# Performance work log

Measured on AMD Instinct MI355X. Metric: run time of the kernel, lower is better.

The kernel has to match this reference:

```python
import jax, jax.numpy as jnp
import numpy as np

P = 131072
S = 64
EMAP_H, EMAP_W = 512, 1024
EPS = 1e-12

def _normalize(x):
    return x / jnp.maximum(jnp.linalg.norm(x, axis=-1, keepdims=True), EPS)

def _construct_tbn(normal):
    # rows = tangent, bitangent, normal -> world-to-local rotation
    up = jnp.broadcast_to(jnp.array([0.0, 1.0, 0.0], normal.dtype), normal.shape)
    tangent = _normalize(jnp.cross(up, normal))
    degen = (normal[..., 0] ** 2 + normal[..., 2] ** 2) <= 0.0
    tangent = jnp.where(degen[..., None], jnp.array([1.0, 0.0, 0.0], normal.dtype), tangent)
    bitangent = _normalize(jnp.cross(normal, tangent))
    return jnp.stack([tangent, bitangent, normal], axis=-2)  # [P,3,3]

def _latlong_uv(d):
    u = 0.5 * (1.0 + jnp.arctan2(d[..., 0], -d[..., 2]) / jnp.pi)
    v = jnp.arccos(jnp.clip(d[..., 1], -1.0, 1.0)) / jnp.pi
    return jnp.stack([u, v], axis=-1)

def _reflect(i, n):
    return _normalize(-i + 2.0 * jnp.sum(i * n, axis=-1, keepdims=True) * n)

def _sample_ggx_vndf(v_local, alpha, u1, u2):
    a3 = jnp.concatenate([alpha, alpha, jnp.ones_like(alpha)], axis=-1)  # [P,3]
    vh = _normalize(v_local * a3)
    ln = jnp.broadcast_to(jnp.array([0.0, 0.0, 1.0], vh.dtype), vh.shape)
    b1 = _normalize(jnp.cross(ln, vh))
    degen = jnp.linalg.norm(vh[:, :2], axis=-1) <= 0.0
    b1 = jnp.where(degen[:, None], jnp.array([1.0, 0.0, 0.0], vh.dtype), b1)
    b2 = _normalize(jnp.cross(vh, b1))
    r = jnp.sqrt(u1)
    theta = 2.0 * jnp.pi * u2
    t1 = r * jnp.cos(theta)
    t2 = r * jnp.sin(theta)
    s = 0.5 * (1.0 + vh[:, 2:3])
    t2 = (1.0 - s) * jnp.sqrt(1.0 - t1 ** 2) + s * t2
    t3 = jnp.sqrt(jnp.clip(1.0 - t1 ** 2 - t2 ** 2, 0.0, 1.0))
    mh = (t1[..., None] * b1[:, None, :] + t2[..., None] * b2[:, None, :]
          + t3[..., None] * vh[:, None, :])
    return _normalize(mh * a3[:, None, :])  # [P,S,3]

def _grid_sample_border(img, grid):
    # img: [3,H,W]; grid: [...,2] in [-1,1]; bilinear, align_corners=False, border pad
    H, W = img.shape[1], img.shape[2]
    x = ((grid[..., 0] + 1.0) * W - 1.0) * 0.5
    y = ((grid[..., 1] + 1.0) * H - 1.0) * 0.5
    x0f = jnp.floor(x); y0f = jnp.floor(y)
    wx = x - x0f; wy = y - y0f
    x0 = jnp.clip(x0f.astype(jnp.int32), 0, W - 1)
    x1 = jnp.clip(x0f.astype(jnp.int32) + 1, 0, W - 1)
    y0 = jnp.clip(y0f.astype(jnp.int32), 0, H - 1)
    y1 = jnp.clip(y0f.astype(jnp.int32) + 1, 0, H - 1)
    v00 = img[:, y0, x0]; v01 = img[:, y0, x1]
    v10 = img[:, y1, x0]; v11 = img[:, y1, x1]
    out = (v00 * (1 - wx) * (1 - wy) + v01 * wx * (1 - wy)
           + v10 * (1 - wx) * wy + v11 * wx * wy)
    return jnp.moveaxis(out, 0, -1)  # [...,3]

def _smith(alpha, cos):
    a2 = alpha ** 2
    return 2.0 * cos / (cos + jnp.sqrt(a2 + (1.0 - a2) * cos ** 2))

def _forward(emap, view_dir, normal, albedo, roughness, metalness, u1, u2, uc, vc):
    img = emap[0]  # [3,H,W]
    alpha = roughness ** 2
    tbn = _construct_tbn(normal)  # [P,3,3]
    v_local = jnp.einsum('pij,pj->pi', tbn, view_dir)
    m_local = _sample_ggx_vndf(v_local, alpha, u1, u2)       # [P,S,3]
    m_world = jnp.einsum('pji,psj->psi', tbn, m_local)       # tbn^T @ m
    light = _reflect(view_dir[:, None, :], m_world)          # [P,S,3]
    rad = _grid_sample_border(img, _latlong_uv(light) * 2.0 - 1.0)  # [P,S,3]
    # specular (metal) shading
    half = _normalize(view_dir[:, None, :] + light)
    hdv = jnp.clip(jnp.sum(half * view_dir[:, None, :], axis=-1), 0.0, 1.0)
    ndv = jnp.clip(jnp.sum(normal[:, None, :] * view_dir[:, None, :], axis=-1), 0.0, 1.0)
    ndl = jnp.clip(jnp.sum(normal[:, None, :] * light, axis=-1), 0.0, 1.0)
    f0 = metalness * albedo + (1.0 - metalness) * 0.04       # [P,3]
    fresnel = f0[:, None, :] + (1.0 - f0[:, None, :]) * (1.0 - hdv[..., None]) ** 5
    geometric = _smith(alpha, ndv) * _smith(alpha, ndl)
    smith_view = jnp.clip(_smith(alpha, ndv), 1e-10, 1.0)
    spec = jnp.mean(fresnel * geometric[..., None] * rad / smith_view[..., None], axis=1)
    # diffuse: cosine-hemisphere sampling + Lambert
    phi = 2.0 * jnp.pi * uc
    ct = jnp.sqrt(vc); st = jnp.sqrt(1.0 - vc)
    ld_local = jnp.stack([jnp.cos(phi) * st, jnp.sin(phi) * st, ct], axis=-1)
    ld = jnp.einsum('pji,psj->psi', tbn, ld_local)
    rad_d = _grid_sample_border(img, _latlong_uv(ld) * 2.0 - 1.0)
    kd = albedo * (1.0 - metalness)
    diff = jnp.mean(rad_d * kd[:, None, :], axis=1)
    return spec + diff  # [P,3]

def setup_inputs() -> dict:
    key = jax.random.key(0)
    ks = jax.random.split(key, 10)
    view_dir = _normalize(jax.random.normal(ks[0], (P, 3), jnp.float32))
    normal = _normalize(jax.random.normal(ks[1], (P, 3), jnp.float32))
    albedo = jax.random.uniform(ks[2], (P, 3), jnp.float32)
    roughness = 0.05 + 0.9 * jax.random.uniform(ks[3], (P, 1), jnp.float32)
    metalness = jax.random.uniform(ks[4], (P, 1), jnp.float32)
    emap = jax.random.uniform(ks[5], (1, 3, EMAP_H, EMAP_W), jnp.float32) * 2.0
    u1 = jax.random.uniform(ks[6], (P, S), jnp.float32)
    u2 = jax.random.uniform(ks[7], (P, S), jnp.float32)
    uc = jax.random.uniform(ks[8], (P, S), jnp.float32)
    vc = jax.random.uniform(ks[9], (P, S), jnp.float32)
    return {"emap": emap, "view_dir": view_dir, "normal": normal, "albedo": albedo,
            "roughness": roughness, "metalness": metalness,
            "u1": u1, "u2": u2, "uc": uc, "vc": vc}

def reference(emap, view_dir, normal, albedo, roughness, metalness, u1, u2, uc, vc):
    return _forward(emap, view_dir, normal, albedo, roughness, metalness, u1, u2, uc, vc)
```

## Files before the change

### kernel.cpp

```cpp
#include <hip/hip_runtime.h>
#include <math.h>

namespace {

constexpr int PN = 131072;
constexpr int SN = 64;
constexpr int EH = 512;
constexpr int EW = 1024;
constexpr float SPI = 162.97466172610083f;

struct F3 { float x, y, z; };

__device__ __forceinline__ float dot3(F3 a, F3 b) { return a.x*b.x + a.y*b.y + a.z*b.z; }
__device__ __forceinline__ F3 cross3(F3 a, F3 b) {
    return F3{a.y*b.z - a.z*b.y, a.z*b.x - a.x*b.z, a.x*b.y - a.y*b.x};
}
__device__ __forceinline__ float clampf(float x, float lo, float hi) {
    return fminf(fmaxf(x, lo), hi);
}
__device__ __forceinline__ F3 norm3(F3 a) {
    float l2 = a.x*a.x + a.y*a.y + a.z*a.z;
    float inv = __builtin_amdgcn_rsqf(fmaxf(l2, 1e-24f));
    return F3{a.x*inv, a.y*inv, a.z*inv};
}
__device__ __forceinline__ float smithf(float alpha, float c) {
    float a2 = alpha*alpha;
    float den = c + __builtin_amdgcn_sqrtf(a2 + (1.0f - a2)*c*c);
    return 2.0f*c*__builtin_amdgcn_rcpf(den);
}

__device__ __forceinline__ float fast_atan2(float y, float x) {
    float ax = fabsf(x), ay = fabsf(y);
    float mx = fmaxf(ax, ay), mn = fminf(ax, ay);
    float a = mn * __builtin_amdgcn_rcpf(mx);
    if (mx == 0.0f) a = 0.0f;
    float s = a*a;
    float p = fmaf(s, -0.01172120f, 0.05265332f);
    p = fmaf(s, p, -0.11643287f);
    p = fmaf(s, p,  0.19354346f);
    p = fmaf(s, p, -0.33262347f);
    p = fmaf(s, p,  0.99997726f);
    float r = p * a;
    if (ay > ax)  r = 1.57079632679f - r;
    if (x < 0.0f) r = 3.14159265359f - r;
    return copysignf(r, y);
}

__device__ __forceinline__ float fast_acos(float x) {
    float ax = fabsf(x);
    float p = fmaf(ax, -0.0012624911f, 0.0066700901f);
    p = fmaf(ax, p, -0.0170881256f);
    p = fmaf(ax, p,  0.0308918810f);
    p = fmaf(ax, p, -0.0501743046f);
    p = fmaf(ax, p,  0.0889789874f);
    p = fmaf(ax, p, -0.2145988016f);
    p = fmaf(ax, p,  1.5707963050f);
    float s = __builtin_amdgcn_sqrtf(fmaxf(1.0f - ax, 0.0f));
    float r = s * p;
    return (x >= 0.0f) ? r : 3.14159265359f - r;
}

__device__ __forceinline__ void env_addr(F3 d, int& i0, int& i1,
                                         float& wx, float& wy,
                                         bool& at_l, bool& at_r) {
    float t  = fast_atan2(d.x, -d.z);
    float vv = fast_acos(clampf(d.y, -1.0f, 1.0f));
    float x = fmaf(t,  SPI, 511.5f);
    float y = fmaf(vv, SPI, -0.5f);
    float x0f = floorf(x), y0f = floorf(y);
    wx = x - x0f; wy = y - y0f;
    int ix = (int)x0f, iy = (int)y0f;
    int xb = min(max(ix, 0), EW - 2);
    int y0 = min(max(iy, 0), EH - 1);
    int y1 = min(max(iy + 1, 0), EH - 1);
    at_l = ix < 0;
    at_r = ix >= EW - 1;
    i0 = (y0 << 10) + xb;
    i1 = (y1 << 10) + xb;
}

__device__ __forceinline__ void rgb9e5_addmul(unsigned int v, float w, F3& acc) {
    float scale = __uint_as_float(((v >> 27) + 103u) << 23);
    float ws = w * scale;
    acc.x = fmaf((float)(v & 511u), ws, acc.x);
    acc.y = fmaf((float)((v >> 9) & 511u), ws, acc.y);
    acc.z = fmaf((float)((v >> 18) & 511u), ws, acc.z);
}

__device__ __forceinline__ F3 env_blend9(uint2 r0, uint2 r1, float wx, float wy,
                                         bool at_l, bool at_r) {
    unsigned int t00 = at_r ? r0.y : r0.x;
    unsigned int t01 = at_l ? r0.x : r0.y;
    unsigned int t10 = at_r ? r1.y : r1.x;
    unsigned int t11 = at_l ? r1.x : r1.y;
    float w00 = (1.0f - wx)*(1.0f - wy);
    float w01 = wx*(1.0f - wy);
    float w10 = (1.0f - wx)*wy;
    float w11 = wx*wy;
    F3 acc{0.0f, 0.0f, 0.0f};
    rgb9e5_addmul(t00, w00, acc);
    rgb9e5_addmul(t01, w01, acc);
    rgb9e5_addmul(t10, w10, acc);
    rgb9e5_addmul(t11, w11, acc);
    return acc;
}

template<int CTRL, int ROW_MASK, bool BC>
__device__ __forceinline__ float dpp_add_step(float x) {
    int ti = __builtin_amdgcn_update_dpp(0, __float_as_int(x), CTRL, ROW_MASK, 0xf, BC);
    return x + __int_as_float(ti);
}
__device__ __forceinline__ float wave_sum(float x) {
    x = dpp_add_step<0x111, 0xf, true >(x);
    x = dpp_add_step<0x112, 0xf, true >(x);
    x = dpp_add_step<0x114, 0xf, true >(x);
    x = dpp_add_step<0x118, 0xf, true >(x);
    x = dpp_add_step<0x142, 0xa, false>(x);
    x = dpp_add_step<0x143, 0xc, false>(x);
    return __int_as_float(__builtin_amdgcn_readlane(__float_as_int(x), 63));
}

__global__ void relayout_kernel(const float* __restrict__ img, unsigned int* __restrict__ tex) {
    int i = blockIdx.x*blockDim.x + threadIdx.x;
    const int HW = EH*EW;
    if (i < HW) {
        float r = img[i], g = img[HW + i], b = img[2*HW + i];
        float m = fmaxf(fmaxf(r, g), b);
        int es = min(max((int)(__float_as_uint(m) >> 23) - 111, 0), 31);
        float sc = __uint_as_float((unsigned int)(151 - es) << 23);
        unsigned int R = min(511u, (unsigned int)rintf(r*sc));
        unsigned int G = min(511u, (unsigned int)rintf(g*sc));
        unsigned int B = min(511u, (unsigned int)rintf(b*sc));
        tex[i] = ((unsigned int)es << 27) | (B << 18) | (G << 9) | R;
    }
}

template<bool TEX>
__global__ __launch_bounds__(256) void ibl_kernel(
    const float* __restrict__ emap, const unsigned int* __restrict__ tex,
    const float* __restrict__ view_dir, const float* __restrict__ normal,
    const float* __restrict__ albedo, const float* __restrict__ rough_,
    const float* __restrict__ metal_, const float* __restrict__ u1_,
    const float* __restrict__ u2_, const float* __restrict__ uc_,
    const float* __restrict__ vc_, float* __restrict__ out)
{
    int lane = threadIdx.x & 63;
    int wid  = (blockIdx.x << 2) + (threadIdx.x >> 6);
    int p0   = __builtin_amdgcn_readfirstlane(wid << 1);

    float U1[2], U2[2], UC[2], VC[2];
    F3 v[2], n[2], f0[2], kd[2];
    float alpha[2];
    #pragma unroll
    for (int k = 0; k < 2; ++k) {
        int p = p0 + k;
        size_t si = (size_t)p*SN + lane;
        U1[k] = __builtin_nontemporal_load(u1_ + si);
        U2[k] = __builtin_nontemporal_load(u2_ + si);
        UC[k] = __builtin_nontemporal_load(uc_ + si);
        VC[k] = __builtin_nontemporal_load(vc_ + si);
        v[k]   = F3{view_dir[3*p], view_dir[3*p+1], view_dir[3*p+2]};
        n[k]   = F3{normal[3*p],   normal[3*p+1],   normal[3*p+2]};
        F3 alb = F3{albedo[3*p],   albedo[3*p+1],   albedo[3*p+2]};
        float rg = rough_[p];
        alpha[k] = rg*rg;
        float metal = metal_[p];
        f0[k] = F3{metal*alb.x + (1.0f - metal)*0.04f,
                   metal*alb.y + (1.0f - metal)*0.04f,
                   metal*alb.z + (1.0f - metal)*0.04f};
        kd[k] = F3{alb.x*(1.0f - metal), alb.y*(1.0f - metal), alb.z*(1.0f - metal)};
    }

    F3 t[2], b[2];
    #pragma unroll
    for (int k = 0; k < 2; ++k) {
        float nx2nz2 = n[k].x*n[k].x + n[k].z*n[k].z;
        if (nx2nz2 <= 0.0f) t[k] = F3{1.0f, 0.0f, 0.0f};
        else                t[k] = norm3(F3{n[k].z, 0.0f, -n[k].x});
        b[k] = cross3(n[k], t[k]);
    }

    uint2 dr0[2], dr1[2];
    float dwx[2], dwy[2];
    bool d_l[2], d_r[2];
    F3 ld[2];
    #pragma unroll
    for (int k = 0; k < 2; ++k) {
        float sph = __builtin_amdgcn_sinf(UC[k]);
        float cph = __builtin_amdgcn_cosf(UC[k]);
        float ct = __builtin_amdgcn_sqrtf(VC[k]);
        float st = __builtin_amdgcn_sqrtf(fmaxf(1.0f - VC[k], 0.0f));
        F3 ldl = F3{cph*st, sph*st, ct};
        ld[k] = F3{t[k].x*ldl.x + b[k].x*ldl.y + n[k].x*ldl.z,
                   t[k].y*ldl.x + b[k].y*ldl.y + n[k].y*ldl.z,
                   t[k].z*ldl.x + b[k].z*ldl.y + n[k].z*ldl.z};
        if (TEX) {
            int i0, i1;
            env_addr(ld[k], i0, i1, dwx[k], dwy[k], d_l[k], d_r[k]);
            dr0[k] = *reinterpret_cast<const uint2*>(tex + i0);
            dr1[k] = *reinterpret_cast<const uint2*>(tex + i1);
        }
    }

    uint2 sr0[2], sr1[2];
    float swx[2], swy[2];
    bool s_l[2], s_r[2];
    F3 light[2];
    float sv_ratio[2];
    #pragma unroll
    for (int k = 0; k < 2; ++k) {
        F3 vl = F3{dot3(t[k], v[k]), dot3(b[k], v[k]), dot3(n[k], v[k])};
        float ndv = clampf(vl.z, 0.0f, 1.0f);
        float s_ndv = smithf(alpha[k], ndv);
        float inv_sv = __builtin_amdgcn_rcpf(clampf(s_ndv, 1e-10f, 1.0f));
        sv_ratio[k] = s_ndv * inv_sv;

        F3 vh = norm3(F3{vl.x*alpha[k], vl.y*alpha[k], vl.z});
        F3 b1;
        float l2d = vh.x*vh.x + vh.y*vh.y;
        if (l2d <= 0.0f) b1 = F3{1.0f, 0.0f, 0.0f};
        else             b1 = norm3(F3{-vh.y, vh.x, 0.0f});
        F3 b2 = cross3(vh, b1);
        float sfac = 0.5f*(1.0f + vh.z);

        float r = __builtin_amdgcn_sqrtf(U1[k]);
        float sth = __builtin_amdgcn_sinf(U2[k]);
        float cth = __builtin_amdgcn_cosf(U2[k]);
        float t1 = r*cth;
        float t2 = r*sth;
        t2 = (1.0f - sfac)*__builtin_amdgcn_sqrtf(fmaxf(1.0f - t1*t1, 0.0f)) + sfac*t2;
        float t3 = __builtin_amdgcn_sqrtf(clampf(1.0f - t1*t1 - t2*t2, 0.0f, 1.0f));
        F3 mh = F3{t1*b1.x + t2*b2.x + t3*vh.x,
                   t1*b1.y + t2*b2.y + t3*vh.y,
                   t1*b1.z + t2*b2.z + t3*vh.z};
        F3 ml = norm3(F3{mh.x*alpha[k], mh.y*alpha[k], mh.z});
        F3 m = F3{t[k].x*ml.x + b[k].x*ml.y + n[k].x*ml.z,
                  t[k].y*ml.x + b[k].y*ml.y + n[k].y*ml.z,
                  t[k].z*ml.x + b[k].z*ml.y + n[k].z*ml.z};
        float idm = dot3(v[k], m);
        light[k] = F3{fmaf(2.0f*idm, m.x, -v[k].x),
                      fmaf(2.0f*idm, m.y, -v[k].y),
                      fmaf(2.0f*idm, m.z, -v[k].z)};
        if (TEX) {
            int i0, i1;
            env_addr(light[k], i0, i1, swx[k], swy[k], s_l[k], s_r[k]);
            sr0[k] = *reinterpret_cast<const uint2*>(tex + i0);
            sr1[k] = *reinterpret_cast<const uint2*>(tex + i1);
        }
    }

    float fresc[2];
    float om5[2];
    #pragma unroll
    for (int k = 0; k < 2; ++k) {
        F3 hlf = norm3(F3{v[k].x + light[k].x, v[k].y + light[k].y, v[k].z + light[k].z});
        float hdv = clampf(dot3(hlf, v[k]), 0.0f, 1.0f);
        float ndl = clampf(dot3(n[k], light[k]), 0.0f, 1.0f);
        float s_ndl = smithf(alpha[k], ndl);
        fresc[k] = sv_ratio[k] * s_ndl;
        float om = 1.0f - hdv;
        float om2 = om*om;
        om5[k] = om2*om2*om;
    }

    #pragma unroll
    for (int k = 0; k < 2; ++k) {
        F3 rad, radd;
        if (TEX) {
            radd = env_blend9(dr0[k], dr1[k], dwx[k], dwy[k], d_l[k], d_r[k]);
            rad  = env_blend9(sr0[k], sr1[k], swx[k], swy[k], s_l[k], s_r[k]);
        } else {
            const int HW = EH*EW;
            #pragma unroll
            for (int pass = 0; pass < 2; ++pass) {
                F3 d = pass ? light[k] : ld[k];
                int i0, i1; float wx, wy; bool atl, atr;
                env_addr(d, i0, i1, wx, wy, atl, atr);
                int x0 = atr ? 1 : 0, x1 = atl ? 0 : 1;
                F3 o;
                float* po = &o.x;
                #pragma unroll
                for (int c = 0; c < 3; ++c) {
                    const float* pl = emap + c*HW;
                    float v00 = pl[i0 + x0], v01 = pl[i0 + x1];
                    float v10 = pl[i1 + x0], v11 = pl[i1 + x1];
                    float rr0 = fmaf(wx, v01 - v00, v00);
                    float rr1 = fmaf(wx, v11 - v10, v10);
                    po[c] = fmaf(wy, rr1 - rr0, rr0);
                }
                if (pass) rad = o; else radd = o;
            }
        }
        float gs = fresc[k];
        F3 acc;
        acc.x = fmaf((f0[k].x + (1.0f - f0[k].x)*om5[k])*gs, rad.x, radd.x*kd[k].x);
        acc.y = fmaf((f0[k].y + (1.0f - f0[k].y)*om5[k])*gs, rad.y, radd.y*kd[k].y);
        acc.z = fmaf((f0[k].z + (1.0f - f0[k].z)*om5[k])*gs, rad.z, radd.z*kd[k].z);

        float sx = wave_sum(acc.x);
        float sy = wave_sum(acc.y);
        float sz = wave_sum(acc.z);

        if (lane == 0) {
            const float inv_s = 1.0f/(float)SN;
            int p = p0 + k;
            __builtin_nontemporal_store(sx*inv_s, out + 3*p + 0);
            __builtin_nontemporal_store(sy*inv_s, out + 3*p + 1);
            __builtin_nontemporal_store(sz*inv_s, out + 3*p + 2);
        }
    }
}

}

extern "C" void kernel_launch(void* const* d_in, const int* in_sizes, int n_in,
                              void* d_out, int out_size, void* d_ws, size_t ws_size,
                              hipStream_t stream) {
    const float* emap     = (const float*)d_in[0];
    const float* view_dir = (const float*)d_in[1];
    const float* normal   = (const float*)d_in[2];
    const float* albedo   = (const float*)d_in[3];
    const float* rough    = (const float*)d_in[4];
    const float* metal    = (const float*)d_in[5];
    const float* u1       = (const float*)d_in[6];
    const float* u2       = (const float*)d_in[7];
    const float* uc       = (const float*)d_in[8];
    const float* vc       = (const float*)d_in[9];
    float* out            = (float*)d_out;

    const int HW = EH*EW;
    const size_t tex_bytes = (size_t)HW*sizeof(unsigned int);
    const int main_blocks = PN/8;

    if (ws_size >= tex_bytes) {
        unsigned int* tex = (unsigned int*)d_ws;
        relayout_kernel<<<(HW + 255)/256, 256, 0, stream>>>(emap, tex);
        ibl_kernel<true><<<main_blocks, 256, 0, stream>>>(
            emap, tex, view_dir, normal, albedo, rough, metal, u1, u2, uc, vc, out);
    } else {
        ibl_kernel<false><<<main_blocks, 256, 0, stream>>>(
            emap, nullptr, view_dir, normal, albedo, rough, metal, u1, u2, uc, vc, out);
    }
}
```

Baseline: 153.5 us.

## Process four points per wave and simplify shading math

Each wave now handles four points instead of two, which halves the grid size and gives more independent texture gathers in flight per wave to hide memory latency. The half-vector normalization is replaced by a closed-form half-angle identity, the Smith ratio clamp is turned into a select, and tangent normalization uses one rsq. The wave reduction now writes from lane 63 instead of doing a readlane, and f0/kd are computed late to shorten register live ranges. More points per wave raises register pressure and may cut occupancy.

```diff
diff --git a/kernel.cpp b/kernel.cpp
--- a/kernel.cpp
+++ b/kernel.cpp
@@ -7,6 +7,7 @@
 constexpr int SN = 64;
 constexpr int EH = 512;
 constexpr int EW = 1024;
+constexpr int KP = 4;
 constexpr float SPI = 162.97466172610083f;
 
 struct F3 { float x, y, z; };
@@ -110,14 +111,14 @@
     int ti = __builtin_amdgcn_update_dpp(0, __float_as_int(x), CTRL, ROW_MASK, 0xf, BC);
     return x + __int_as_float(ti);
 }
-__device__ __forceinline__ float wave_sum(float x) {
+__device__ __forceinline__ float wave_sum63(float x) {
     x = dpp_add_step<0x111, 0xf, true >(x);
     x = dpp_add_step<0x112, 0xf, true >(x);
     x = dpp_add_step<0x114, 0xf, true >(x);
     x = dpp_add_step<0x118, 0xf, true >(x);
     x = dpp_add_step<0x142, 0xa, false>(x);
     x = dpp_add_step<0x143, 0xc, false>(x);
-    return __int_as_float(__builtin_amdgcn_readlane(__float_as_int(x), 63));
+    return x;
 }
 
 __global__ void relayout_kernel(const float* __restrict__ img, unsigned int* __restrict__ tex) {
@@ -146,13 +147,13 @@
 {
     int lane = threadIdx.x & 63;
     int wid  = (blockIdx.x << 2) + (threadIdx.x >> 6);
-    int p0   = __builtin_amdgcn_readfirstlane(wid << 1);
-
-    float U1[2], U2[2], UC[2], VC[2];
-    F3 v[2], n[2], f0[2], kd[2];
-    float alpha[2];
-    #pragma unroll
-    for (int k = 0; k < 2; ++k) {
+    int p0   = __builtin_amdgcn_readfirstlane(wid * KP);
+
+    float U1[KP], U2[KP], UC[KP], VC[KP];
+    F3 v[KP], n[KP], alb[KP];
+    float alpha[KP], metal[KP];
+    #pragma unroll
+    for (int k = 0; k < KP; ++k) {
         int p = p0 + k;
         size_t si = (size_t)p*SN + lane;
         U1[k] = __builtin_nontemporal_load(u1_ + si);
@@ -161,31 +162,28 @@
         VC[k] = __builtin_nontemporal_load(vc_ + si);
         v[k]   = F3{view_dir[3*p], view_dir[3*p+1], view_dir[3*p+2]};
         n[k]   = F3{normal[3*p],   normal[3*p+1],   normal[3*p+2]};
-        F3 alb = F3{albedo[3*p],   albedo[3*p+1],   albedo[3*p+2]};
+        alb[k] = F3{albedo[3*p],   albedo[3*p+1],   albedo[3*p+2]};
         float rg = rough_[p];
         alpha[k] = rg*rg;
-        float metal = metal_[p];
-        f0[k] = F3{metal*alb.x + (1.0f - metal)*0.04f,
-                   metal*alb.y + (1.0f - metal)*0.04f,
-                   metal*alb.z + (1.0f - metal)*0.04f};
-        kd[k] = F3{alb.x*(1.0f - metal), alb.y*(1.0f - metal), alb.z*(1.0f - metal)};
-    }
-
-    F3 t[2], b[2];
-    #pragma unroll
-    for (int k = 0; k < 2; ++k) {
+        metal[k] = metal_[p];
+    }
+
+    F3 t[KP], b[KP];
+    #pragma unroll
+    for (int k = 0; k < KP; ++k) {
         float nx2nz2 = n[k].x*n[k].x + n[k].z*n[k].z;
+        float invt = __builtin_amdgcn_rsqf(nx2nz2);
         if (nx2nz2 <= 0.0f) t[k] = F3{1.0f, 0.0f, 0.0f};
-        else                t[k] = norm3(F3{n[k].z, 0.0f, -n[k].x});
+        else                t[k] = F3{n[k].z*invt, 0.0f, -n[k].x*invt};
         b[k] = cross3(n[k], t[k]);
     }
 
-    uint2 dr0[2], dr1[2];
-    float dwx[2], dwy[2];
-    bool d_l[2], d_r[2];
-    F3 ld[2];
-    #pragma unroll
-    for (int k = 0; k < 2; ++k) {
+    uint2 dr0[KP], dr1[KP];
+    float dwx[KP], dwy[KP];
+    bool d_l[KP], d_r[KP];
+    F3 ld[KP];
+    #pragma unroll
+    for (int k = 0; k < KP; ++k) {
         float sph = __builtin_amdgcn_sinf(UC[k]);
         float cph = __builtin_amdgcn_cosf(UC[k]);
         float ct = __builtin_amdgcn_sqrtf(VC[k]);
@@ -202,24 +200,24 @@
         }
     }
 
-    uint2 sr0[2], sr1[2];
-    float swx[2], swy[2];
-    bool s_l[2], s_r[2];
-    F3 light[2];
-    float sv_ratio[2];
-    #pragma unroll
-    for (int k = 0; k < 2; ++k) {
+    uint2 sr0[KP], sr1[KP];
+    float swx[KP], swy[KP];
+    bool s_l[KP], s_r[KP];
+    F3 light[KP];
+    float sv_ratio[KP];
+    #pragma unroll
+    for (int k = 0; k < KP; ++k) {
         F3 vl = F3{dot3(t[k], v[k]), dot3(b[k], v[k]), dot3(n[k], v[k])};
         float ndv = clampf(vl.z, 0.0f, 1.0f);
         float s_ndv = smithf(alpha[k], ndv);
-        float inv_sv = __builtin_amdgcn_rcpf(clampf(s_ndv, 1e-10f, 1.0f));
-        sv_ratio[k] = s_ndv * inv_sv;
+        sv_ratio[k] = (s_ndv >= 1e-10f) ? 1.0f : s_ndv * 1e10f;
 
         F3 vh = norm3(F3{vl.x*alpha[k], vl.y*alpha[k], vl.z});
         F3 b1;
         float l2d = vh.x*vh.x + vh.y*vh.y;
+        float invb = __builtin_amdgcn_rsqf(l2d);
         if (l2d <= 0.0f) b1 = F3{1.0f, 0.0f, 0.0f};
-        else             b1 = norm3(F3{-vh.y, vh.x, 0.0f});
+        else             b1 = F3{-vh.y*invb, vh.x*invb, 0.0f};
         F3 b2 = cross3(vh, b1);
         float sfac = 0.5f*(1.0f + vh.z);
 
@@ -249,12 +247,12 @@
         }
     }
 
-    float fresc[2];
-    float om5[2];
-    #pragma unroll
-    for (int k = 0; k < 2; ++k) {
-        F3 hlf = norm3(F3{v[k].x + light[k].x, v[k].y + light[k].y, v[k].z + light[k].z});
-        float hdv = clampf(dot3(hlf, v[k]), 0.0f, 1.0f);
+    float fresc[KP];
+    float om5[KP];
+    #pragma unroll
+    for (int k = 0; k < KP; ++k) {
+        float c = dot3(v[k], light[k]);
+        float hdv = __builtin_amdgcn_sqrtf(clampf(0.5f + 0.5f*c, 0.0f, 1.0f));
         float ndl = clampf(dot3(n[k], light[k]), 0.0f, 1.0f);
         float s_ndl = smithf(alpha[k], ndl);
         fresc[k] = sv_ratio[k] * s_ndl;
@@ -264,7 +262,7 @@
     }
 
     #pragma unroll
-    for (int k = 0; k < 2; ++k) {
+    for (int k = 0; k < KP; ++k) {
         F3 rad, radd;
         if (TEX) {
             radd = env_blend9(dr0[k], dr1[k], dwx[k], dwy[k], d_l[k], d_r[k]);
@@ -292,16 +290,21 @@
             }
         }
         float gs = fresc[k];
+        float mt = metal[k];
+        F3 f0 = F3{mt*alb[k].x + (1.0f - mt)*0.04f,
+                   mt*alb[k].y + (1.0f - mt)*0.04f,
+                   mt*alb[k].z + (1.0f - mt)*0.04f};
+        F3 kd = F3{alb[k].x*(1.0f - mt), alb[k].y*(1.0f - mt), alb[k].z*(1.0f - mt)};
         F3 acc;
-        acc.x = fmaf((f0[k].x + (1.0f - f0[k].x)*om5[k])*gs, rad.x, radd.x*kd[k].x);
-        acc.y = fmaf((f0[k].y + (1.0f - f0[k].y)*om5[k])*gs, rad.y, radd.y*kd[k].y);
-        acc.z = fmaf((f0[k].z + (1.0f - f0[k].z)*om5[k])*gs, rad.z, radd.z*kd[k].z);
-
-        float sx = wave_sum(acc.x);
-        float sy = wave_sum(acc.y);
-        float sz = wave_sum(acc.z);
-
-        if (lane == 0) {
+        acc.x = fmaf((f0.x + (1.0f - f0.x)*om5[k])*gs, rad.x, radd.x*kd.x);
+        acc.y = fmaf((f0.y + (1.0f - f0.y)*om5[k])*gs, rad.y, radd.y*kd.y);
+        acc.z = fmaf((f0.z + (1.0f - f0.z)*om5[k])*gs, rad.z, radd.z*kd.z);
+
+        float sx = wave_sum63(acc.x);
+        float sy = wave_sum63(acc.y);
+        float sz = wave_sum63(acc.z);
+
+        if (lane == 63) {
             const float inv_s = 1.0f/(float)SN;
             int p = p0 + k;
             __builtin_nontemporal_store(sx*inv_s, out + 3*p + 0);
@@ -330,7 +333,7 @@
 
     const int HW = EH*EW;
     const size_t tex_bytes = (size_t)HW*sizeof(unsigned int);
-    const int main_blocks = PN/8;
+    const int main_blocks = PN/(4*KP);
 
     if (ws_size >= tex_bytes) {
         unsigned int* tex = (unsigned int*)d_ws;
```

Result: slower. 160.5 us (+4.6%).

## Split fused IBL kernel into separate diffuse and specular passes

Applied to the files above, without the earlier changes.

Splits the single fused kernel into a diffuse kernel that writes the output and a specular kernel that adds into it, so each pass uses fewer registers and has a smaller texture working set. It also simplifies math: the half-vector dot product is computed via the cosine half-angle identity, the shadowing ratio is made branchy instead of using a reciprocal, and the wave reduction reads its result from lane 63 directly, dropping the readlane. The cost is a second launch, per-point inputs (normal, albedo, metal) being reloaded, and a read-modify-write of the output.

```diff
diff --git a/kernel.cpp b/kernel.cpp
--- a/kernel.cpp
+++ b/kernel.cpp
@@ -105,19 +105,38 @@
     return acc;
 }
 
+__device__ __forceinline__ F3 env_sample_f32(const float* __restrict__ emap, F3 d) {
+    const int HW = EH*EW;
+    int i0, i1; float wx, wy; bool atl, atr;
+    env_addr(d, i0, i1, wx, wy, atl, atr);
+    int x0 = atr ? 1 : 0, x1 = atl ? 0 : 1;
+    F3 o;
+    float* po = &o.x;
+    #pragma unroll
+    for (int c = 0; c < 3; ++c) {
+        const float* pl = emap + c*HW;
+        float v00 = pl[i0 + x0], v01 = pl[i0 + x1];
+        float v10 = pl[i1 + x0], v11 = pl[i1 + x1];
+        float rr0 = fmaf(wx, v01 - v00, v00);
+        float rr1 = fmaf(wx, v11 - v10, v10);
+        po[c] = fmaf(wy, rr1 - rr0, rr0);
+    }
+    return o;
+}
+
 template<int CTRL, int ROW_MASK, bool BC>
 __device__ __forceinline__ float dpp_add_step(float x) {
     int ti = __builtin_amdgcn_update_dpp(0, __float_as_int(x), CTRL, ROW_MASK, 0xf, BC);
     return x + __int_as_float(ti);
 }
-__device__ __forceinline__ float wave_sum(float x) {
+__device__ __forceinline__ float wave_sum63(float x) {
     x = dpp_add_step<0x111, 0xf, true >(x);
     x = dpp_add_step<0x112, 0xf, true >(x);
     x = dpp_add_step<0x114, 0xf, true >(x);
     x = dpp_add_step<0x118, 0xf, true >(x);
     x = dpp_add_step<0x142, 0xa, false>(x);
     x = dpp_add_step<0x143, 0xc, false>(x);
-    return __int_as_float(__builtin_amdgcn_readlane(__float_as_int(x), 63));
+    return x;
 }
 
 __global__ void relayout_kernel(const float* __restrict__ img, unsigned int* __restrict__ tex) {
@@ -136,70 +155,103 @@
 }
 
 template<bool TEX>
-__global__ __launch_bounds__(256) void ibl_kernel(
+__global__ __launch_bounds__(256) void diff_kernel(
     const float* __restrict__ emap, const unsigned int* __restrict__ tex,
-    const float* __restrict__ view_dir, const float* __restrict__ normal,
-    const float* __restrict__ albedo, const float* __restrict__ rough_,
-    const float* __restrict__ metal_, const float* __restrict__ u1_,
-    const float* __restrict__ u2_, const float* __restrict__ uc_,
+    const float* __restrict__ normal, const float* __restrict__ albedo,
+    const float* __restrict__ metal_, const float* __restrict__ uc_,
     const float* __restrict__ vc_, float* __restrict__ out)
 {
     int lane = threadIdx.x & 63;
     int wid  = (blockIdx.x << 2) + (threadIdx.x >> 6);
     int p0   = __builtin_amdgcn_readfirstlane(wid << 1);
 
-    float U1[2], U2[2], UC[2], VC[2];
-    F3 v[2], n[2], f0[2], kd[2];
-    float alpha[2];
+    float UC[2], VC[2];
+    F3 n[2], kd[2];
     #pragma unroll
     for (int k = 0; k < 2; ++k) {
         int p = p0 + k;
         size_t si = (size_t)p*SN + lane;
-        U1[k] = __builtin_nontemporal_load(u1_ + si);
-        U2[k] = __builtin_nontemporal_load(u2_ + si);
         UC[k] = __builtin_nontemporal_load(uc_ + si);
         VC[k] = __builtin_nontemporal_load(vc_ + si);
-        v[k]   = F3{view_dir[3*p], view_dir[3*p+1], view_dir[3*p+2]};
-        n[k]   = F3{normal[3*p],   normal[3*p+1],   normal[3*p+2]};
-        F3 alb = F3{albedo[3*p],   albedo[3*p+1],   albedo[3*p+2]};
-        float rg = rough_[p];
-        alpha[k] = rg*rg;
-        float metal = metal_[p];
-        f0[k] = F3{metal*alb.x + (1.0f - metal)*0.04f,
-                   metal*alb.y + (1.0f - metal)*0.04f,
-                   metal*alb.z + (1.0f - metal)*0.04f};
-        kd[k] = F3{alb.x*(1.0f - metal), alb.y*(1.0f - metal), alb.z*(1.0f - metal)};
-    }
-
-    F3 t[2], b[2];
-    #pragma unroll
-    for (int k = 0; k < 2; ++k) {
-        float nx2nz2 = n[k].x*n[k].x + n[k].z*n[k].z;
-        if (nx2nz2 <= 0.0f) t[k] = F3{1.0f, 0.0f, 0.0f};
-        else                t[k] = norm3(F3{n[k].z, 0.0f, -n[k].x});
-        b[k] = cross3(n[k], t[k]);
+        n[k] = F3{normal[3*p], normal[3*p+1], normal[3*p+2]};
+        float mt = metal_[p];
+        kd[k] = F3{albedo[3*p]*(1.0f - mt), albedo[3*p+1]*(1.0f - mt),
+                   albedo[3*p+2]*(1.0f - mt)};
     }
 
     uint2 dr0[2], dr1[2];
     float dwx[2], dwy[2];
     bool d_l[2], d_r[2];
-    F3 ld[2];
-    #pragma unroll
-    for (int k = 0; k < 2; ++k) {
+    F3 ldv[2];
+    #pragma unroll
+    for (int k = 0; k < 2; ++k) {
+        F3 t;
+        float nx2nz2 = n[k].x*n[k].x + n[k].z*n[k].z;
+        float invt = __builtin_amdgcn_rsqf(nx2nz2);
+        if (nx2nz2 <= 0.0f) t = F3{1.0f, 0.0f, 0.0f};
+        else                t = F3{n[k].z*invt, 0.0f, -n[k].x*invt};
+        F3 b = cross3(n[k], t);
+
         float sph = __builtin_amdgcn_sinf(UC[k]);
         float cph = __builtin_amdgcn_cosf(UC[k]);
         float ct = __builtin_amdgcn_sqrtf(VC[k]);
         float st = __builtin_amdgcn_sqrtf(fmaxf(1.0f - VC[k], 0.0f));
         F3 ldl = F3{cph*st, sph*st, ct};
-        ld[k] = F3{t[k].x*ldl.x + b[k].x*ldl.y + n[k].x*ldl.z,
-                   t[k].y*ldl.x + b[k].y*ldl.y + n[k].y*ldl.z,
-                   t[k].z*ldl.x + b[k].z*ldl.y + n[k].z*ldl.z};
+        ldv[k] = F3{t.x*ldl.x + b.x*ldl.y + n[k].x*ldl.z,
+                    t.y*ldl.x + b.y*ldl.y + n[k].y*ldl.z,
+                    t.z*ldl.x + b.z*ldl.y + n[k].z*ldl.z};
         if (TEX) {
             int i0, i1;
-            env_addr(ld[k], i0, i1, dwx[k], dwy[k], d_l[k], d_r[k]);
+            env_addr(ldv[k], i0, i1, dwx[k], dwy[k], d_l[k], d_r[k]);
             dr0[k] = *reinterpret_cast<const uint2*>(tex + i0);
             dr1[k] = *reinterpret_cast<const uint2*>(tex + i1);
         }
+    }
+
+    #pragma unroll
+    for (int k = 0; k < 2; ++k) {
+        F3 radd = TEX ? env_blend9(dr0[k], dr1[k], dwx[k], dwy[k], d_l[k], d_r[k])
+                      : env_sample_f32(emap, ldv[k]);
+        float sx = wave_sum63(radd.x*kd[k].x);
+        float sy = wave_sum63(radd.y*kd[k].y);
+        float sz = wave_sum63(radd.z*kd[k].z);
+        if (lane == 63) {
+            const float inv_s = 1.0f/(float)SN;
+            int p = p0 + k;
+            out[3*p + 0] = sx*inv_s;
+            out[3*p + 1] = sy*inv_s;
+            out[3*p + 2] = sz*inv_s;
+        }
+    }
+}
+
+template<bool TEX>
+__global__ __launch_bounds__(256) void spec_kernel(
+    const float* __restrict__ emap, const unsigned int* __restrict__ tex,
+    const float* __restrict__ view_dir, const float* __restrict__ normal,
+    const float* __restrict__ albedo, const float* __restrict__ rough_,
+    const float* __restrict__ metal_, const float* __restrict__ u1_,
+    const float* __restrict__ u2_, float* __restrict__ out)
+{
+    int lane = threadIdx.x & 63;
+    int wid  = (blockIdx.x << 2) + (threadIdx.x >> 6);
+    int p0   = __builtin_amdgcn_readfirstlane(wid << 1);
+
+    float U1[2], U2[2];
+    F3 v[2], n[2], alb[2];
+    float alpha[2], metal[2];
+    #pragma unroll
+    for (int k = 0; k < 2; ++k) {
+        int p = p0 + k;
+        size_t si = (size_t)p*SN + lane;
+        U1[k] = __builtin_nontemporal_load(u1_ + si);
+        U2[k] = __builtin_nontemporal_load(u2_ + si);
+        v[k]   = F3{view_dir[3*p], view_dir[3*p+1], view_dir[3*p+2]};
+        n[k]   = F3{normal[3*p],   normal[3*p+1],   normal[3*p+2]};
+        alb[k] = F3{albedo[3*p],   albedo[3*p+1],   albedo[3*p+2]};
+        float rg = rough_[p];
+        alpha[k] = rg*rg;
+        metal[k] = metal_[p];
     }
 
     uint2 sr0[2], sr1[2];
@@ -207,19 +259,27 @@
     bool s_l[2], s_r[2];
     F3 light[2];
     float sv_ratio[2];
-    #pragma unroll
-    for (int k = 0; k < 2; ++k) {
-        F3 vl = F3{dot3(t[k], v[k]), dot3(b[k], v[k]), dot3(n[k], v[k])};
+    F3 nv[2];
+    #pragma unroll
+    for (int k = 0; k < 2; ++k) {
+        F3 t;
+        float nx2nz2 = n[k].x*n[k].x + n[k].z*n[k].z;
+        float invt = __builtin_amdgcn_rsqf(nx2nz2);
+        if (nx2nz2 <= 0.0f) t = F3{1.0f, 0.0f, 0.0f};
+        else                t = F3{n[k].z*invt, 0.0f, -n[k].x*invt};
+        F3 b = cross3(n[k], t);
+
+        F3 vl = F3{dot3(t, v[k]), dot3(b, v[k]), dot3(n[k], v[k])};
         float ndv = clampf(vl.z, 0.0f, 1.0f);
         float s_ndv = smithf(alpha[k], ndv);
-        float inv_sv = __builtin_amdgcn_rcpf(clampf(s_ndv, 1e-10f, 1.0f));
-        sv_ratio[k] = s_ndv * inv_sv;
+        sv_ratio[k] = (s_ndv >= 1e-10f) ? 1.0f : s_ndv * 1e10f;
 
         F3 vh = norm3(F3{vl.x*alpha[k], vl.y*alpha[k], vl.z});
         F3 b1;
         float l2d = vh.x*vh.x + vh.y*vh.y;
+        float invb = __builtin_amdgcn_rsqf(l2d);
         if (l2d <= 0.0f) b1 = F3{1.0f, 0.0f, 0.0f};
-        else             b1 = norm3(F3{-vh.y, vh.x, 0.0f});
+        else             b1 = F3{-vh.y*invb, vh.x*invb, 0.0f};
         F3 b2 = cross3(vh, b1);
         float sfac = 0.5f*(1.0f + vh.z);
 
@@ -234,9 +294,9 @@
                    t1*b1.y + t2*b2.y + t3*vh.y,
                    t1*b1.z + t2*b2.z + t3*vh.z};
         F3 ml = norm3(F3{mh.x*alpha[k], mh.y*alpha[k], mh.z});
-        F3 m = F3{t[k].x*ml.x + b[k].x*ml.y + n[k].x*ml.z,
-                  t[k].y*ml.x + b[k].y*ml.y + n[k].y*ml.z,
-                  t[k].z*ml.x + b[k].z*ml.y + n[k].z*ml.z};
+        F3 m = F3{t.x*ml.x + b.x*ml.y + n[k].x*ml.z,
+                  t.y*ml.x + b.y*ml.y + n[k].y*ml.z,
+                  t.z*ml.x + b.z*ml.y + n[k].z*ml.z};
         float idm = dot3(v[k], m);
         light[k] = F3{fmaf(2.0f*idm, m.x, -v[k].x),
                       fmaf(2.0f*idm, m.y, -v[k].y),
@@ -249,15 +309,14 @@
         }
     }
 
-    float fresc[2];
-    float om5[2];
-    #pragma unroll
-    for (int k = 0; k < 2; ++k) {
-        F3 hlf = norm3(F3{v[k].x + light[k].x, v[k].y + light[k].y, v[k].z + light[k].z});
-        float hdv = clampf(dot3(hlf, v[k]), 0.0f, 1.0f);
+    float gs[2], om5[2];
+    #pragma unroll
+    for (int k = 0; k < 2; ++k) {
+        float c = dot3(v[k], light[k]);
+        float hdv = __builtin_amdgcn_sqrtf(clampf(0.5f + 0.5f*c, 0.0f, 1.0f));
         float ndl = clampf(dot3(n[k], light[k]), 0.0f, 1.0f);
         float s_ndl = smithf(alpha[k], ndl);
-        fresc[k] = sv_ratio[k] * s_ndl;
+        gs[k] = sv_ratio[k] * s_ndl;
         float om = 1.0f - hdv;
         float om2 = om*om;
         om5[k] = om2*om2*om;
@@ -265,48 +324,21 @@
 
     #pragma unroll
     for (int k = 0; k < 2; ++k) {
-        F3 rad, radd;
-        if (TEX) {
-            radd = env_blend9(dr0[k], dr1[k], dwx[k], dwy[k], d_l[k], d_r[k]);
-            rad  = env_blend9(sr0[k], sr1[k], swx[k], swy[k], s_l[k], s_r[k]);
-        } else {
-            const int HW = EH*EW;
-            #pragma unroll
-            for (int pass = 0; pass < 2; ++pass) {
-                F3 d = pass ? light[k] : ld[k];
-                int i0, i1; float wx, wy; bool atl, atr;
-                env_addr(d, i0, i1, wx, wy, atl, atr);
-                int x0 = atr ? 1 : 0, x1 = atl ? 0 : 1;
-                F3 o;
-                float* po = &o.x;
-                #pragma unroll
-                for (int c = 0; c < 3; ++c) {
-                    const float* pl = emap + c*HW;
-                    float v00 = pl[i0 + x0], v01 = pl[i0 + x1];
-                    float v10 = pl[i1 + x0], v11 = pl[i1 + x1];
-                    float rr0 = fmaf(wx, v01 - v00, v00);
-                    float rr1 = fmaf(wx, v11 - v10, v10);
-                    po[c] = fmaf(wy, rr1 - rr0, rr0);
-                }
-                if (pass) rad = o; else radd = o;
-            }
-        }
-        float gs = fresc[k];
-        F3 acc;
-        acc.x = fmaf((f0[k].x + (1.0f - f0[k].x)*om5[k])*gs, rad.x, radd.x*kd[k].x);
-        acc.y = fmaf((f0[k].y + (1.0f - f0[k].y)*om5[k])*gs, rad.y, radd.y*kd[k].y);
-        acc.z = fmaf((f0[k].z + (1.0f - f0[k].z)*om5[k])*gs, rad.z, radd.z*kd[k].z);
-
-        float sx = wave_sum(acc.x);
-        float sy = wave_sum(acc.y);
-        float sz = wave_sum(acc.z);
-
-        if (lane == 0) {
+        F3 rad = TEX ? env_blend9(sr0[k], sr1[k], swx[k], swy[k], s_l[k], s_r[k])
+                     : env_sample_f32(emap, light[k]);
+        float mt = metal[k];
+        F3 f0 = F3{mt*alb[k].x + (1.0f - mt)*0.04f,
+                   mt*alb[k].y + (1.0f - mt)*0.04f,
+                   mt*alb[k].z + (1.0f - mt)*0.04f};
+        float sx = wave_sum63((f0.x + (1.0f - f0.x)*om5[k])*gs[k]*rad.x);
+        float sy = wave_sum63((f0.y + (1.0f - f0.y)*om5[k])*gs[k]*rad.y);
+        float sz = wave_sum63((f0.z + (1.0f - f0.z)*om5[k])*gs[k]*rad.z);
+        if (lane == 63) {
             const float inv_s = 1.0f/(float)SN;
             int p = p0 + k;
-            __builtin_nontemporal_store(sx*inv_s, out + 3*p + 0);
-            __builtin_nontemporal_store(sy*inv_s, out + 3*p + 1);
-            __builtin_nontemporal_store(sz*inv_s, out + 3*p + 2);
+            out[3*p + 0] += sx*inv_s;
+            out[3*p + 1] += sy*inv_s;
+            out[3*p + 2] += sz*inv_s;
         }
     }
 }
@@ -335,10 +367,14 @@
     if (ws_size >= tex_bytes) {
         unsigned int* tex = (unsigned int*)d_ws;
         relayout_kernel<<<(HW + 255)/256, 256, 0, stream>>>(emap, tex);
-        ibl_kernel<true><<<main_blocks, 256, 0, stream>>>(
-            emap, tex, view_dir, normal, albedo, rough, metal, u1, u2, uc, vc, out);
+        diff_kernel<true><<<main_blocks, 256, 0, stream>>>(
+            emap, tex, normal, albedo, metal, uc, vc, out);
+        spec_kernel<true><<<main_blocks, 256, 0, stream>>>(
+            emap, tex, view_dir, normal, albedo, rough, metal, u1, u2, out);
     } else {
-        ibl_kernel<false><<<main_blocks, 256, 0, stream>>>(
-            emap, nullptr, view_dir, normal, albedo, rough, metal, u1, u2, uc, vc, out);
-    }
-}
+        diff_kernel<false><<<main_blocks, 256, 0, stream>>>(
+            emap, nullptr, normal, albedo, metal, uc, vc, out);
+        spec_kernel<false><<<main_blocks, 256, 0, stream>>>(
+            emap, nullptr, view_dir, normal, albedo, rough, metal, u1, u2, out);
+    }
+}
```

Result: slower. 164.6 us (+7.2%).
